# Kernel optimization log

Measured on AMD Instinct MI355X. Metric: run time of the kernel, lower is better.

The kernel has to match this reference:

```python
import jax, jax.numpy as jnp
import numpy as np


def _conv(x, w, pad):
    return jax.lax.conv_general_dilated(
        x, w, (1, 1), [(pad, pad), (pad, pad)],
        dimension_numbers=('NCHW', 'OIHW', 'NCHW'))


def _avgpool2(x):
    B, C, H, W = x.shape
    return x.reshape(B, C, H // 2, 2, W // 2, 2).mean(axis=(3, 5))


def setup_inputs() -> dict:
    key = jax.random.key(0)
    ks = jax.random.split(key, 10)
    B = 1024
    x = jax.random.uniform(ks[0], (B, 1, 28, 28), jnp.float32)
    # depthwise-separable conv params (in=1 -> depthwise is a plain 3x3 conv)
    dw_w = jax.random.normal(ks[1], (1, 1, 3, 3), jnp.float32) * 0.3
    pw_w = jax.random.normal(ks[2], (32, 1, 1, 1), jnp.float32) * 0.3
    pw_b = jax.random.normal(ks[3], (32,), jnp.float32) * 0.05
    # fixed 4-qubit entangling unitary (real orthogonal 16x16), stand-in for tq.RandomLayer(n_ops=8)
    U = jnp.asarray(np.linalg.qr(np.random.default_rng(0).standard_normal((16, 16)))[0],
                    jnp.float32)
    fus_w = jax.random.normal(ks[4], (128, 36, 3, 3), jnp.float32) * (1.0 / np.sqrt(36 * 9))
    fus_b = jax.random.normal(ks[5], (128,), jnp.float32) * 0.05
    F = 128 * 7 * 7
    cls_w = jax.random.normal(ks[6], (10, F), jnp.float32) * (1.0 / np.sqrt(F))
    cls_b = jax.random.normal(ks[7], (10,), jnp.float32) * 0.05
    reg_w = jax.random.normal(ks[8], (1, F), jnp.float32) * (1.0 / np.sqrt(F))
    reg_b = jax.random.normal(ks[9], (1,), jnp.float32) * 0.05
    return {'x': x, 'dw_w': dw_w, 'pw_w': pw_w, 'pw_b': pw_b, 'U': U,
            'fus_w': fus_w, 'fus_b': fus_b, 'cls_w': cls_w, 'cls_b': cls_b,
            'reg_w': reg_w, 'reg_b': reg_b}


def _quantum_patches(x, U):
    # x: (B,1,28,28) -> 14x14 grid of 2x2 patches, 4 RY angles per patch
    B = x.shape[0]
    p = x.reshape(B, 14, 2, 14, 2).transpose(0, 1, 3, 2, 4).reshape(B, 14, 14, 4)
    h = 0.5 * p
    a = jnp.stack([jnp.cos(h), jnp.sin(h)], axis=-1)       # (B,14,14,4,2)
    # RY-encoded product state |psi> = kron over 4 wires -> 16 real amplitudes
    amp = jnp.einsum('...i,...j,...k,...l->...ijkl',
                     a[..., 0, :], a[..., 1, :], a[..., 2, :], a[..., 3, :]
                     ).reshape(B, 14, 14, 16)
    state = amp @ U.T                                       # entangling layer
    probs = state * state
    idx = jnp.arange(16)
    # PauliZ expectation per wire; wire 0 is the most significant bit
    signs = 1.0 - 2.0 * (((idx[None, :] >> (3 - jnp.arange(4)[:, None])) & 1)
                         .astype(jnp.float32))              # (4,16)
    meas = probs @ signs.T                                  # (B,14,14,4)
    # replicate torch.cat(patches,dim=1).view(B,4,14,14): flat row-major then reshape
    return meas.reshape(B, 14 * 14 * 4).reshape(B, 4, 14, 14)


def reference(x, dw_w, pw_w, pw_b, U, fus_w, fus_b, cls_w, cls_b, reg_w, reg_b):
    B = x.shape[0]
    out_ds = _conv(_conv(x, dw_w, 1), pw_w, 0) + pw_b[None, :, None, None]  # (B,32,28,28)
    out_q = _quantum_patches(x, U)                                          # (B,4,14,14)
    out = jnp.concatenate([_avgpool2(out_ds), out_q], axis=1)               # (B,36,14,14)
    out = jax.nn.relu(_conv(out, fus_w, 1) + fus_b[None, :, None, None])    # (B,128,14,14)
    out = _avgpool2(out)                                                    # (B,128,7,7)
    flat = out.reshape(B, -1)
    logits = flat @ cls_w.T + cls_b
    aux = flat @ reg_w.T + reg_b
    return (logits, aux)
```

## Files before the change

### kernel.cpp

```cpp
#include <hip/hip_runtime.h>
#include <math.h>


typedef __bf16 bf16x8 __attribute__((ext_vector_type(8)));
typedef __bf16 bf16x4 __attribute__((ext_vector_type(4)));
typedef float  f32x16 __attribute__((ext_vector_type(16)));

union Pack8 { __bf16 h[8]; uint4 v; };
union QPair { struct { bf16x4 lo, hi; } p; bf16x8 v; };

__global__ __launch_bounds__(256) void prep(
    const float* __restrict__ fus_w,
    const float* __restrict__ cls_w,
    const float* __restrict__ reg_w,
    __bf16* __restrict__ bfrag,
    float* __restrict__ clsTT)
{
    const int gid = blockIdx.x * 256 + threadIdx.x;
    if (gid < 43008) {
        const int j    = gid & 7;
        const int frag = gid >> 3;
        const int lane = frag & 63;
        const int rest = frag >> 6;
        const int m  = rest % 21;
        const int nt = rest / 21;
        const int n  = nt * 32 + (lane & 31);
        const int hk = lane >> 5;
        float v;
        if (m < 18) {
            const int t = m >> 1, ks = m & 1;
            const int ic = ks * 16 + hk * 8 + j;
            v = fus_w[n * 324 + ic * 9 + t];
        } else {
            const int ps = m - 18;
            const int k  = hk * 8 + j;
            const int tap = ps * 4 + (k >> 2);
            const int ch  = k & 3;
            v = (tap < 9) ? fus_w[n * 324 + (32 + ch) * 9 + tap] : 0.f;
        }
        bfrag[gid] = (__bf16)v;
    } else if (gid < 43008 + 86016) {
        const int e   = gid - 43008;
        const int kk  = e % 12;
        const int r0  = e / 12;
        const int l31 = r0 & 31;
        const int r1  = r0 >> 5;
        const int hk  = r1 & 1;
        const int r2  = r1 >> 1;
        const int q   = r2 & 3;
        const int r3  = r2 >> 2;
        const int mt  = r3 % 7;
        const int nt  = r3 / 7;
        const int oc   = nt * 32 + l31;
        const int cell = mt * 8 + q * 2 + hk;
        float v = 0.f;
        if (cell < 49 && kk < 11) {
            const int f = oc * 49 + cell;
            v = (kk < 10) ? cls_w[kk * 6272 + f] : reg_w[f];
        }
        clsTT[e] = v;
    }
}

__device__ __forceinline__ void patch_work(
    const int p, const float* __restrict__ xs, __bf16* __restrict__ actT,
    __bf16* __restrict__ Qt,
    const float* __restrict__ dw_w, const float* __restrict__ pw_w,
    const float* __restrict__ pw_b, const float* __restrict__ U)
{
    if (p >= 196) return;
    const int i = p / 14, j = p % 14;
    const int Y = 2 * i, X = 2 * j;

    float w9[9];
    #pragma unroll
    for (int t = 0; t < 9; ++t) w9[t] = dw_w[t];
    float dsum = 0.f;
    #pragma unroll
    for (int dy = 0; dy < 2; ++dy) {
        #pragma unroll
        for (int dx = 0; dx < 2; ++dx) {
            const int cy = Y + dy, cx = X + dx;
            #pragma unroll
            for (int ky = 0; ky < 3; ++ky) {
                const int yy = cy + ky - 1;
                if (yy < 0 || yy > 27) continue;
                #pragma unroll
                for (int kx = 0; kx < 3; ++kx) {
                    const int xx = cx + kx - 1;
                    if (xx < 0 || xx > 27) continue;
                    dsum += xs[yy * 29 + xx] * w9[ky * 3 + kx];
                }
            }
        }
    }
    const float dpool = 0.25f * dsum;

    const int sp_o = (i + 1) * 16 + (j + 1);
    #pragma unroll
    for (int c8 = 0; c8 < 4; ++c8) {
        Pack8 pk;
        #pragma unroll
        for (int e = 0; e < 8; ++e)
            pk.h[e] = (__bf16)(pw_w[c8 * 8 + e] * dpool + pw_b[c8 * 8 + e]);
        ((uint4*)actT)[sp_o * 5 + c8] = pk.v;
    }

    const float p0 = xs[Y * 29 + X],       p1 = xs[Y * 29 + X + 1];
    const float p2 = xs[(Y + 1) * 29 + X], p3 = xs[(Y + 1) * 29 + X + 1];
    float c0, s0, c1, s1, c2, s2, c3, s3;
    sincosf(0.5f * p0, &s0, &c0);
    sincosf(0.5f * p1, &s1, &c1);
    sincosf(0.5f * p2, &s2, &c2);
    sincosf(0.5f * p3, &s3, &c3);
    float a01[4] = {c0 * c1, c0 * s1, s0 * c1, s0 * s1};
    float a23[4] = {c2 * c3, c2 * s3, s2 * c3, s2 * s3};
    float amp[16];
    #pragma unroll
    for (int hi = 0; hi < 4; ++hi)
        #pragma unroll
        for (int lo = 0; lo < 4; ++lo)
            amp[hi * 4 + lo] = a01[hi] * a23[lo];

    float meas[4] = {0.f, 0.f, 0.f, 0.f};
    #pragma unroll
    for (int m = 0; m < 16; ++m) {
        float st = 0.f;
        #pragma unroll
        for (int n = 0; n < 16; ++n) st = fmaf(U[m * 16 + n], amp[n], st);
        const float pm = st * st;
        meas[0] += ((m >> 3) & 1) ? -pm : pm;
        meas[1] += ((m >> 2) & 1) ? -pm : pm;
        meas[2] += ((m >> 1) & 1) ? -pm : pm;
        meas[3] += (m & 1) ? -pm : pm;
    }
    const int fbase = i * 56 + j * 4;
    #pragma unroll
    for (int w = 0; w < 4; ++w) {
        const int f  = fbase + w;
        const int ch = f / 196;
        const int sp = f - ch * 196;
        const int r2 = sp / 14 + 1, c2i = sp % 14 + 1;
        const int sp2 = r2 * 16 + c2i;
        Qt[sp2 * 4 + ch] = (__bf16)meas[w];
    }
}

__device__ __forceinline__ void conv_fold(
    const __bf16* __restrict__ actT, const __bf16* __restrict__ Qt,
    const bf16x8* __restrict__ bfr, const float4* __restrict__ cls4,
    const float fb_l, const int l31, const int hk,
    const int* __restrict__ offL, const int* __restrict__ offH,
    float* __restrict__ a11)
{
    for (int mt = 0; mt < 7; ++mt) {
        const int mp   = mt * 32 + l31;
        const int cell = mp >> 2;
        const int cc = (cell < 49) ? cell : 48;
        const int py = (cc * 9363) >> 16;
        const int px = cc - py * 7;
        const int yy = 2 * py + ((mp >> 1) & 1);
        const int xx = 2 * px + (mp & 1);
        const int rowbase = yy * 16 + xx;

        f32x16 acc = {0.f,0.f,0.f,0.f,0.f,0.f,0.f,0.f,
                      0.f,0.f,0.f,0.f,0.f,0.f,0.f,0.f};

        #pragma unroll
        for (int t = 0; t < 9; ++t) {
            const int ky = t / 3, kx = t - ky * 3;
            const int row = rowbase + ky * 16 + kx;
            const __bf16* rp = actT + row * 40 + hk * 8;
            #pragma unroll
            for (int ks = 0; ks < 2; ++ks) {
                const bf16x8 af = *(const bf16x8*)(rp + ks * 16);
                acc = __builtin_amdgcn_mfma_f32_32x32x16_bf16(af, bfr[t * 2 + ks],
                                                              acc, 0, 0, 0);
            }
        }
        #pragma unroll
        for (int ps = 0; ps < 3; ++ps) {
            QPair u;
            u.p.lo = *(const bf16x4*)(Qt + (rowbase + offL[ps]) * 4);
            u.p.hi = *(const bf16x4*)(Qt + (rowbase + offH[ps]) * 4);
            acc = __builtin_amdgcn_mfma_f32_32x32x16_bf16(u.v, bfr[18 + ps],
                                                          acc, 0, 0, 0);
        }

        const float4* cwm = cls4 + mt * 768;
        #pragma unroll
        for (int q = 0; q < 4; ++q) {
            float pv = 0.f;
            #pragma unroll
            for (int s = 0; s < 4; ++s) {
                const float v = acc[q * 4 + s] + fb_l;
                pv += (v > 0.f ? v : 0.f);
            }
            pv *= 0.25f;
            const float4 w0 = cwm[q * 192 + 0];
            const float4 w1 = cwm[q * 192 + 1];
            const float4 w2 = cwm[q * 192 + 2];
            a11[0]  = fmaf(pv, w0.x, a11[0]);
            a11[1]  = fmaf(pv, w0.y, a11[1]);
            a11[2]  = fmaf(pv, w0.z, a11[2]);
            a11[3]  = fmaf(pv, w0.w, a11[3]);
            a11[4]  = fmaf(pv, w1.x, a11[4]);
            a11[5]  = fmaf(pv, w1.y, a11[5]);
            a11[6]  = fmaf(pv, w1.z, a11[6]);
            a11[7]  = fmaf(pv, w1.w, a11[7]);
            a11[8]  = fmaf(pv, w2.x, a11[8]);
            a11[9]  = fmaf(pv, w2.y, a11[9]);
            a11[10] = fmaf(pv, w2.z, a11[10]);
        }
    }
}

__global__ __launch_bounds__(256, 2) void quanv_fused(
    const float* __restrict__ x,
    const float* __restrict__ dw_w,
    const float* __restrict__ pw_w,
    const float* __restrict__ pw_b,
    const float* __restrict__ U,
    const __bf16* __restrict__ bfrag,
    const float* __restrict__ fus_b,
    const float* __restrict__ clsTT,
    const float* __restrict__ cls_b,
    const float* __restrict__ reg_b,
    float* __restrict__ out,
    int B)
{
    __shared__ __align__(16) __bf16 actT[2][256 * 40];
    __shared__ __align__(16) __bf16 Qt[2][256 * 4];
    __shared__ float xs[2][812];
    __shared__ float red[2][48];

    const int b0  = blockIdx.x * 2;
    const int b1  = b0 + 1;
    const bool two = (b1 < B);
    const int tid = threadIdx.x;

    {
        uint4 z; z.x = 0; z.y = 0; z.z = 0; z.w = 0;
        uint4* a4 = (uint4*)&actT[0][0];
        for (int i = tid; i < 2560; i += 256) a4[i] = z;
        uint4* q4 = (uint4*)&Qt[0][0];
        if (tid < 256) q4[tid] = z;
        const float* xb = x + (size_t)b0 * 784;
        const int tot = two ? 1568 : 784;
        for (int i = tid; i < tot; i += 256) {
            const int img = i / 784, r = i - img * 784;
            xs[img][r + r / 28] = xb[i];
        }
    }

    const int lane = tid & 63, nt = tid >> 6;
    const int l31  = lane & 31, hk = lane >> 5;
    const float fb_l = fus_b[nt * 32 + l31];
    const int pidx = (lane < 49) ? nt * 49 + lane : 999;

    bf16x8 bfr[21];
    {
        const bf16x8* __restrict__ bp = ((const bf16x8*)bfrag) + (nt * 21 * 64 + lane);
        #pragma unroll
        for (int m = 0; m < 21; ++m) bfr[m] = bp[m * 64];
    }

    int offL[3], offH[3];
    #pragma unroll
    for (int ps = 0; ps < 3; ++ps) {
        int tL = ps * 4 + hk * 2;
        int tH = tL + 1;
        if (tL > 8) tL = 0;
        if (tH > 8) tH = 0;
        offL[ps] = (tL / 3) * 16 + (tL % 3);
        offH[ps] = (tH / 3) * 16 + (tH % 3);
    }

    const float4* __restrict__ cls4 =
        ((const float4*)clsTT) + ((((nt * 7) * 4) * 2 + hk) * 32 + l31) * 3;

    __syncthreads();

    patch_work(pidx, &xs[0][0], &actT[0][0], &Qt[0][0], dw_w, pw_w, pw_b, U);
    __syncthreads();

    float a11_0[11];
    #pragma unroll
    for (int k = 0; k < 11; ++k) a11_0[k] = 0.f;
    if (two) patch_work(pidx, &xs[1][0], &actT[1][0], &Qt[1][0], dw_w, pw_w, pw_b, U);
    conv_fold(&actT[0][0], &Qt[0][0], bfr, cls4, fb_l, l31, hk, offL, offH, a11_0);
    __syncthreads();

    float a11_1[11];
    #pragma unroll
    for (int k = 0; k < 11; ++k) a11_1[k] = 0.f;
    if (two) conv_fold(&actT[1][0], &Qt[1][0], bfr, cls4, fb_l, l31, hk, offL, offH, a11_1);

    #pragma unroll
    for (int k = 0; k < 11; ++k) {
        float a = a11_0[k];
        float c = a11_1[k];
        #pragma unroll
        for (int off = 32; off > 0; off >>= 1) {
            a += __shfl_down(a, off, 64);
            c += __shfl_down(c, off, 64);
        }
        if (lane == 0) { red[0][k * 4 + nt] = a; red[1][k * 4 + nt] = c; }
    }
    __syncthreads();
    if (tid < 11) {
        const float v = red[0][tid * 4] + red[0][tid * 4 + 1]
                      + red[0][tid * 4 + 2] + red[0][tid * 4 + 3];
        if (tid < 10) out[b0 * 10 + tid] = v + cls_b[tid];
        else          out[B * 10 + b0]   = v + reg_b[0];
    } else if (two && tid >= 64 && tid < 75) {
        const int k = tid - 64;
        const float v = red[1][k * 4] + red[1][k * 4 + 1]
                      + red[1][k * 4 + 2] + red[1][k * 4 + 3];
        if (k < 10) out[b1 * 10 + k] = v + cls_b[k];
        else        out[B * 10 + b1] = v + reg_b[0];
    }
}

extern "C" void kernel_launch(void* const* d_in, const int* in_sizes, int n_in,
                              void* d_out, int out_size, void* d_ws, size_t ws_size,
                              hipStream_t stream) {
    const float* x    = (const float*)d_in[0];
    const float* dw_w = (const float*)d_in[1];
    const float* pw_w = (const float*)d_in[2];
    const float* pw_b = (const float*)d_in[3];
    const float* U    = (const float*)d_in[4];
    const float* fw   = (const float*)d_in[5];
    const float* fb   = (const float*)d_in[6];
    const float* cw   = (const float*)d_in[7];
    const float* cb   = (const float*)d_in[8];
    const float* rw   = (const float*)d_in[9];
    const float* rb   = (const float*)d_in[10];
    const int B = in_sizes[0] / 784;

    __bf16* bfrag = (__bf16*)d_ws;
    float*  clsTT = (float*)((char*)d_ws + 86016);

    prep<<<(43008 + 86016 + 255) / 256, 256, 0, stream>>>(fw, cw, rw, bfrag, clsTT);
    const int nblk = (B + 1) / 2;
    quanv_fused<<<nblk, 256, 0, stream>>>(x, dw_w, pw_w, pw_b, U, bfrag, fb,
                                          clsTT, cb, rb, (float*)d_out, B);
}
```

Before: 108.8 us.

## Split conv MFMA work so each wave computes two N-tiles over half the M-tiles

```diff
diff --git a/kernel.cpp b/kernel.cpp
--- a/kernel.cpp
+++ b/kernel.cpp
@@ -146,14 +146,15 @@
     }
 }
 
-__device__ __forceinline__ void conv_fold(
+__device__ __forceinline__ void conv_fold2(
     const __bf16* __restrict__ actT, const __bf16* __restrict__ Qt,
-    const bf16x8* __restrict__ bfr, const float4* __restrict__ cls4,
-    const float fb_l, const int l31, const int hk,
+    const bf16x8* __restrict__ bfrA, const bf16x8* __restrict__ bfrB,
+    const float4* __restrict__ cls4A, const float4* __restrict__ cls4B,
+    const float fbA, const float fbB, const int l31, const int hk,
     const int* __restrict__ offL, const int* __restrict__ offH,
-    float* __restrict__ a11)
+    const int mt0, const int mt1, float* __restrict__ a11)
 {
-    for (int mt = 0; mt < 7; ++mt) {
+    for (int mt = mt0; mt < mt1; ++mt) {
         const int mp   = mt * 32 + l31;
         const int cell = mp >> 2;
         const int cc = (cell < 49) ? cell : 48;
@@ -163,54 +164,69 @@
         const int xx = 2 * px + (mp & 1);
         const int rowbase = yy * 16 + xx;
 
-        f32x16 acc = {0.f,0.f,0.f,0.f,0.f,0.f,0.f,0.f,
-                      0.f,0.f,0.f,0.f,0.f,0.f,0.f,0.f};
+        f32x16 accA = {0.f,0.f,0.f,0.f,0.f,0.f,0.f,0.f,
+                       0.f,0.f,0.f,0.f,0.f,0.f,0.f,0.f};
+        f32x16 accB = {0.f,0.f,0.f,0.f,0.f,0.f,0.f,0.f,
+                       0.f,0.f,0.f,0.f,0.f,0.f,0.f,0.f};
 
         #pragma unroll
         for (int t = 0; t < 9; ++t) {
             const int ky = t / 3, kx = t - ky * 3;
             const int row = rowbase + ky * 16 + kx;
             const __bf16* rp = actT + row * 40 + hk * 8;
-            #pragma unroll
-            for (int ks = 0; ks < 2; ++ks) {
-                const bf16x8 af = *(const bf16x8*)(rp + ks * 16);
-                acc = __builtin_amdgcn_mfma_f32_32x32x16_bf16(af, bfr[t * 2 + ks],
-                                                              acc, 0, 0, 0);
-            }
+            const bf16x8 af0 = *(const bf16x8*)(rp);
+            const bf16x8 af1 = *(const bf16x8*)(rp + 16);
+            accA = __builtin_amdgcn_mfma_f32_32x32x16_bf16(af0, bfrA[t * 2 + 0],
+                                                           accA, 0, 0, 0);
+            accB = __builtin_amdgcn_mfma_f32_32x32x16_bf16(af0, bfrB[t * 2 + 0],
+                                                           accB, 0, 0, 0);
+            accA = __builtin_amdgcn_mfma_f32_32x32x16_bf16(af1, bfrA[t * 2 + 1],
+                                                           accA, 0, 0, 0);
+            accB = __builtin_amdgcn_mfma_f32_32x32x16_bf16(af1, bfrB[t * 2 + 1],
+                                                           accB, 0, 0, 0);
         }
         #pragma unroll
         for (int ps = 0; ps < 3; ++ps) {
             QPair u;
             u.p.lo = *(const bf16x4*)(Qt + (rowbase + offL[ps]) * 4);
             u.p.hi = *(const bf16x4*)(Qt + (rowbase + offH[ps]) * 4);
-            acc = __builtin_amdgcn_mfma_f32_32x32x16_bf16(u.v, bfr[18 + ps],
-                                                          acc, 0, 0, 0);
-        }
-
-        const float4* cwm = cls4 + mt * 768;
+            accA = __builtin_amdgcn_mfma_f32_32x32x16_bf16(u.v, bfrA[18 + ps],
+                                                           accA, 0, 0, 0);
+            accB = __builtin_amdgcn_mfma_f32_32x32x16_bf16(u.v, bfrB[18 + ps],
+                                                           accB, 0, 0, 0);
+        }
+
+        const float4* cwmA = cls4A + mt * 768;
+        const float4* cwmB = cls4B + mt * 768;
         #pragma unroll
         for (int q = 0; q < 4; ++q) {
-            float pv = 0.f;
+            float pvA = 0.f, pvB = 0.f;
             #pragma unroll
             for (int s = 0; s < 4; ++s) {
-                const float v = acc[q * 4 + s] + fb_l;
-                pv += (v > 0.f ? v : 0.f);
+                const float vA = accA[q * 4 + s] + fbA;
+                const float vB = accB[q * 4 + s] + fbB;
+                pvA += (vA > 0.f ? vA : 0.f);
+                pvB += (vB > 0.f ? vB : 0.f);
             }
-            pv *= 0.25f;
-            const float4 w0 = cwm[q * 192 + 0];
-            const float4 w1 = cwm[q * 192 + 1];
-            const float4 w2 = cwm[q * 192 + 2];
-            a11[0]  = fmaf(pv, w0.x, a11[0]);
-            a11[1]  = fmaf(pv, w0.y, a11[1]);
-            a11[2]  = fmaf(pv, w0.z, a11[2]);
-            a11[3]  = fmaf(pv, w0.w, a11[3]);
-            a11[4]  = fmaf(pv, w1.x, a11[4]);
-            a11[5]  = fmaf(pv, w1.y, a11[5]);
-            a11[6]  = fmaf(pv, w1.z, a11[6]);
-            a11[7]  = fmaf(pv, w1.w, a11[7]);
-            a11[8]  = fmaf(pv, w2.x, a11[8]);
-            a11[9]  = fmaf(pv, w2.y, a11[9]);
-            a11[10] = fmaf(pv, w2.z, a11[10]);
+            pvA *= 0.25f;
+            pvB *= 0.25f;
+            const float4 a0 = cwmA[q * 192 + 0];
+            const float4 a1 = cwmA[q * 192 + 1];
+            const float4 a2 = cwmA[q * 192 + 2];
+            const float4 b0 = cwmB[q * 192 + 0];
+            const float4 b1 = cwmB[q * 192 + 1];
+            const float4 b2 = cwmB[q * 192 + 2];
+            a11[0]  = fmaf(pvA, a0.x, fmaf(pvB, b0.x, a11[0]));
+            a11[1]  = fmaf(pvA, a0.y, fmaf(pvB, b0.y, a11[1]));
+            a11[2]  = fmaf(pvA, a0.z, fmaf(pvB, b0.z, a11[2]));
+            a11[3]  = fmaf(pvA, a0.w, fmaf(pvB, b0.w, a11[3]));
+            a11[4]  = fmaf(pvA, a1.x, fmaf(pvB, b1.x, a11[4]));
+            a11[5]  = fmaf(pvA, a1.y, fmaf(pvB, b1.y, a11[5]));
+            a11[6]  = fmaf(pvA, a1.z, fmaf(pvB, b1.z, a11[6]));
+            a11[7]  = fmaf(pvA, a1.w, fmaf(pvB, b1.w, a11[7]));
+            a11[8]  = fmaf(pvA, a2.x, fmaf(pvB, b2.x, a11[8]));
+            a11[9]  = fmaf(pvA, a2.y, fmaf(pvB, b2.y, a11[9]));
+            a11[10] = fmaf(pvA, a2.z, fmaf(pvB, b2.z, a11[10]));
         }
     }
 }
@@ -253,16 +269,22 @@
         }
     }
 
-    const int lane = tid & 63, nt = tid >> 6;
+    const int lane = tid & 63, wv = tid >> 6;
+    const int np   = wv & 1;
+    const int mh   = wv >> 1;
+    const int mt0  = mh ? 4 : 0, mt1 = mh ? 7 : 4;
+    const int ntA  = np * 2, ntB = np * 2 + 1;
     const int l31  = lane & 31, hk = lane >> 5;
-    const float fb_l = fus_b[nt * 32 + l31];
-    const int pidx = (lane < 49) ? nt * 49 + lane : 999;
-
-    bf16x8 bfr[21];
+    const float fbA = fus_b[ntA * 32 + l31];
+    const float fbB = fus_b[ntB * 32 + l31];
+    const int pidx = (lane < 49) ? wv * 49 + lane : 999;
+
+    bf16x8 bfrA[21], bfrB[21];
     {
-        const bf16x8* __restrict__ bp = ((const bf16x8*)bfrag) + (nt * 21 * 64 + lane);
-        #pragma unroll
-        for (int m = 0; m < 21; ++m) bfr[m] = bp[m * 64];
+        const bf16x8* __restrict__ bpA = ((const bf16x8*)bfrag) + (ntA * 21 * 64 + lane);
+        const bf16x8* __restrict__ bpB = ((const bf16x8*)bfrag) + (ntB * 21 * 64 + lane);
+        #pragma unroll
+        for (int m = 0; m < 21; ++m) { bfrA[m] = bpA[m * 64]; bfrB[m] = bpB[m * 64]; }
     }
 
     int offL[3], offH[3];
@@ -276,8 +298,10 @@
         offH[ps] = (tH / 3) * 16 + (tH % 3);
     }
 
-    const float4* __restrict__ cls4 =
-        ((const float4*)clsTT) + ((((nt * 7) * 4) * 2 + hk) * 32 + l31) * 3;
+    const float4* __restrict__ cls4A =
+        ((const float4*)clsTT) + ((((ntA * 7) * 4) * 2 + hk) * 32 + l31) * 3;
+    const float4* __restrict__ cls4B =
+        ((const float4*)clsTT) + ((((ntB * 7) * 4) * 2 + hk) * 32 + l31) * 3;
 
     __syncthreads();
 
@@ -288,13 +312,16 @@
     #pragma unroll
     for (int k = 0; k < 11; ++k) a11_0[k] = 0.f;
     if (two) patch_work(pidx, &xs[1][0], &actT[1][0], &Qt[1][0], dw_w, pw_w, pw_b, U);
-    conv_fold(&actT[0][0], &Qt[0][0], bfr, cls4, fb_l, l31, hk, offL, offH, a11_0);
+    conv_fold2(&actT[0][0], &Qt[0][0], bfrA, bfrB, cls4A, cls4B, fbA, fbB,
+               l31, hk, offL, offH, mt0, mt1, a11_0);
     __syncthreads();
 
     float a11_1[11];
     #pragma unroll
     for (int k = 0; k < 11; ++k) a11_1[k] = 0.f;
-    if (two) conv_fold(&actT[1][0], &Qt[1][0], bfr, cls4, fb_l, l31, hk, offL, offH, a11_1);
+    if (two)
+        conv_fold2(&actT[1][0], &Qt[1][0], bfrA, bfrB, cls4A, cls4B, fbA, fbB,
+                   l31, hk, offL, offH, mt0, mt1, a11_1);
 
     #pragma unroll
     for (int k = 0; k < 11; ++k) {
@@ -305,7 +332,7 @@
             a += __shfl_down(a, off, 64);
             c += __shfl_down(c, off, 64);
         }
-        if (lane == 0) { red[0][k * 4 + nt] = a; red[1][k * 4 + nt] = c; }
+        if (lane == 0) { red[0][k * 4 + wv] = a; red[1][k * 4 + wv] = c; }
     }
     __syncthreads();
     if (tid < 11) {
```

Result: slower. 124.2 us (+14.1%).
